# Performance work log

Hardware: AMD Instinct MI355X
Metric: run time of the kernel (lower is better)

The kernel has to match this reference:

```python
import jax, jax.numpy as jnp
import numpy as np

V, E, P, NL, H, I = 50304, 512, 320, 6, 8, 1024
B, S = 2, 1024
HD = P // H            # head_dim = 40
ROT = int(HD * 0.25)   # rotary dims = 10


def layer_norm(x, w, b, eps=1e-5):
    m = jnp.mean(x, -1, keepdims=True)
    v = jnp.mean((x - m) ** 2, -1, keepdims=True)
    return (x - m) * jax.lax.rsqrt(v + eps) * w + b


def setup_inputs() -> dict:
    key = jax.random.key(0)
    ks = jax.random.split(key, 16)
    n = lambda k, s: jax.random.normal(k, s, dtype=jnp.float32) * 0.02
    return dict(
        input_ids=jax.random.randint(ks[0], (B, S), 0, V),
        embed_w=n(ks[1], (V, E)),
        embed_norm_w=jnp.ones((E,)), embed_norm_b=jnp.zeros((E,)),
        dproj_w=n(ks[2], (P + E, P)), dproj_b=jnp.zeros((P,)),
        dproj_ln_w=jnp.ones((P,)), dproj_ln_b=jnp.zeros((P,)),
        ln1_w=jnp.ones((NL, P)), ln1_b=jnp.zeros((NL, P)),
        ln2_w=jnp.ones((NL, P)), ln2_b=jnp.zeros((NL, P)),
        qkv_w=n(ks[3], (NL, P, 3 * P)), qkv_b=jnp.zeros((NL, 3 * P)),
        dense_w=n(ks[4], (NL, P, P)), dense_b=jnp.zeros((NL, P)),
        fc1_w=n(ks[5], (NL, P, I)), fc1_b=jnp.zeros((NL, I)),
        fc2_w=n(ks[6], (NL, I, P)), fc2_b=jnp.zeros((NL, P)),
        final_ln_w=jnp.ones((P,)), final_ln_b=jnp.zeros((P,)),
        lm_head_w=n(ks[7], (V, P)),
    )


def _forward(input_ids, embed_w, embed_norm_w, embed_norm_b, dproj_w, dproj_b,
             dproj_ln_w, dproj_ln_b, ln1_w, ln1_b, ln2_w, ln2_b, qkv_w, qkv_b,
             dense_w, dense_b, fc1_w, fc1_b, fc2_w, fc2_b, final_ln_w, final_ln_b,
             lm_head_w):
    b, s = input_ids.shape
    # 1-2) token embedding + LayerNorm
    te = layer_norm(embed_w[input_ids], embed_norm_w, embed_norm_b)  # [B,S,E]

    # 3) sequential DiverseProjection recurrence over seq_len (lax.scan)
    def step(prev, emb_t):  # prev [B,P], emb_t [B,E]
        h = jnp.concatenate([prev, emb_t], -1) @ dproj_w + dproj_b
        h = jnp.tanh(layer_norm(h, dproj_ln_w, dproj_ln_b))
        return h, h
    _, hs = jax.lax.scan(step, jnp.zeros((b, P), te.dtype), jnp.swapaxes(te, 0, 1))
    x = jnp.swapaxes(hs, 0, 1)  # [B,S,P]

    # RoPE tables (GPT-NeoX style, rotary_pct = 0.25 of head_dim)
    half = ROT // 2
    inv = 1.0 / (10000.0 ** (jnp.arange(0, ROT, 2, dtype=jnp.float32) / ROT))
    freqs = jnp.arange(s, dtype=jnp.float32)[:, None] * inv[None, :]  # [S, ROT/2]
    cos = jnp.cos(jnp.concatenate([freqs, freqs], -1))  # [S, ROT]
    sin = jnp.sin(jnp.concatenate([freqs, freqs], -1))

    def rope(t):  # t: [B,H,S,ROT]
        t1, t2 = t[..., :half], t[..., half:]
        return t * cos + jnp.concatenate([-t2, t1], -1) * sin

    mask = jnp.tril(jnp.ones((s, s), dtype=bool))
    scale = 1.0 / np.sqrt(HD)
    # 4) Pythia (GPT-NeoX) layers: parallel residual attn + mlp
    for l in range(NL):
        a_in = layer_norm(x, ln1_w[l], ln1_b[l])
        qkv = (a_in @ qkv_w[l] + qkv_b[l]).reshape(b, s, H, 3 * HD)
        q, k, v = (jnp.swapaxes(t, 1, 2) for t in jnp.split(qkv, 3, axis=-1))  # [B,H,S,HD]
        q = jnp.concatenate([rope(q[..., :ROT]), q[..., ROT:]], -1)
        k = jnp.concatenate([rope(k[..., :ROT]), k[..., ROT:]], -1)
        scores = jnp.einsum('bhqd,bhkd->bhqk', q, k) * scale
        attn = jax.nn.softmax(jnp.where(mask, scores, jnp.float32(-1e9)), axis=-1)
        ctx = jnp.einsum('bhqk,bhkd->bhqd', attn, v)
        attn_out = jnp.swapaxes(ctx, 1, 2).reshape(b, s, P) @ dense_w[l] + dense_b[l]
        m_in = layer_norm(x, ln2_w[l], ln2_b[l])
        mlp_out = jax.nn.gelu(m_in @ fc1_w[l] + fc1_b[l]) @ fc2_w[l] + fc2_b[l]
        x = x + attn_out + mlp_out
    # 5-6) final LN + LM head (no bias)
    x = layer_norm(x, final_ln_w, final_ln_b)
    return x @ lm_head_w.T  # [B,S,V]


def reference(input_ids, embed_w, embed_norm_w, embed_norm_b, dproj_w, dproj_b,
              dproj_ln_w, dproj_ln_b, ln1_w, ln1_b, ln2_w, ln2_b, qkv_w, qkv_b,
              dense_w, dense_b, fc1_w, fc1_b, fc2_w, fc2_b, final_ln_w, final_ln_b,
              lm_head_w):
    return _forward(input_ids, embed_w, embed_norm_w, embed_norm_b, dproj_w, dproj_b,
                    dproj_ln_w, dproj_ln_b, ln1_w, ln1_b, ln2_w, ln2_b, qkv_w, qkv_b,
                    dense_w, dense_b, fc1_w, fc1_b, fc2_w, fc2_b, final_ln_w,
                    final_ln_b, lm_head_w)
```

## Files before the change

### kernel.cpp

```cpp
#include <hip/hip_runtime.h>

#define VV 50304
#define EE 512
#define PP 320
#define NL 6
#define NH 8
#define II 1024
#define BB 2
#define SS 1024
#define HDD 40

typedef __attribute__((ext_vector_type(8))) __bf16 bf16x8;
typedef __attribute__((ext_vector_type(4))) float f32x4;

__device__ __forceinline__ float gelu_tanh(float x) {
    float x3 = x * x * x;
    return 0.5f * x * (1.f + tanhf(0.7978845608028654f * (x + 0.044715f * x3)));
}

template<int CTRL>
__device__ __forceinline__ float dpp_reduce_add(float v) {
    int s = __builtin_amdgcn_update_dpp(0, __builtin_bit_cast(int, v), CTRL, 0xF, 0xF, true);
    return v + __builtin_bit_cast(float, s);
}
#define DPPRED16(x) do { \
    x = dpp_reduce_add<0xB1>(x);   \
    x = dpp_reduce_add<0x4E>(x);   \
    x = dpp_reduce_add<0x141>(x);  \
    x = dpp_reduce_add<0x140>(x);  \
} while (0)

__global__ __launch_bounds__(64) void embed_ln_kernel(
    const int* __restrict__ ids, const float* __restrict__ embed,
    const float* __restrict__ w, const float* __restrict__ b, float* __restrict__ out)
{
    int r = blockIdx.x;
    int lane = threadIdx.x;
    long id = ids[r];
    const float* xr = embed + id * (long)EE;
    float vals[8];
    float s = 0.f;
#pragma unroll
    for (int i = 0; i < 8; ++i) { vals[i] = xr[lane + i * 64]; s += vals[i]; }
#pragma unroll
    for (int m = 32; m >= 1; m >>= 1) s += __shfl_xor(s, m);
    float mean = s * (1.f / 512.f);
    float v = 0.f;
#pragma unroll
    for (int i = 0; i < 8; ++i) { float d = vals[i] - mean; v += d * d; }
#pragma unroll
    for (int m = 32; m >= 1; m >>= 1) v += __shfl_xor(v, m);
    float rstd = rsqrtf(v * (1.f / 512.f) + 1e-5f);
    float* orow = out + (long)r * EE;
#pragma unroll
    for (int i = 0; i < 8; ++i) {
        int c = lane + i * 64;
        orow[c] = (vals[i] - mean) * rstd * w[c] + b[c];
    }
}

__global__ __launch_bounds__(64) void ln_kernel(
    const float* __restrict__ x, const float* __restrict__ w,
    const float* __restrict__ b, float* __restrict__ out, int N)
{
    int r = blockIdx.x, lane = threadIdx.x;
    const float* xr = x + (long)r * N;
    float s = 0.f;
    for (int i = lane; i < N; i += 64) s += xr[i];
#pragma unroll
    for (int m = 32; m >= 1; m >>= 1) s += __shfl_xor(s, m);
    float mean = s / (float)N;
    float v = 0.f;
    for (int i = lane; i < N; i += 64) { float d = xr[i] - mean; v += d * d; }
#pragma unroll
    for (int m = 32; m >= 1; m >>= 1) v += __shfl_xor(v, m);
    float rstd = rsqrtf(v / (float)N + 1e-5f);
    float* orow = out + (long)r * N;
    for (int i = lane; i < N; i += 64) orow[i] = (xr[i] - mean) * rstd * w[i] + b[i];
}

__global__ __launch_bounds__(256) void gemm_kernel(
    const float* __restrict__ A, const float* __restrict__ B,
    const float* __restrict__ bias, float* __restrict__ C,
    int M, int N, int K, int BT, int act,
    const float* __restrict__ add1, const float* __restrict__ add2)
{
    __shared__ __align__(16) __bf16 As[64 * 40];
    __shared__ __align__(16) __bf16 Bs[64 * 40];
    int tid  = threadIdx.x;
    int lane = tid & 63;
    int wv   = tid >> 6;
    int l15  = lane & 15, quad = lane >> 4;
    int bm = blockIdx.y * 64, bn = blockIdx.x * 64;
    int wm = (wv >> 1) * 32, wn = (wv & 1) * 32;
    f32x4 acc[2][2] = {};

    int sm = tid >> 2;
    int sk = (tid & 3) * 8;
    int bk_n = tid & 63;
    int bk_k = (tid >> 6) * 8;

    for (int k0 = 0; k0 < K; k0 += 32) {
        {
            const float* ap = A + (long)(bm + sm) * K + k0 + sk;
            float4 a0 = *(const float4*)ap;
            float4 a1 = *(const float4*)(ap + 4);
            bf16x8 av;
            av[0] = (__bf16)a0.x; av[1] = (__bf16)a0.y; av[2] = (__bf16)a0.z; av[3] = (__bf16)a0.w;
            av[4] = (__bf16)a1.x; av[5] = (__bf16)a1.y; av[6] = (__bf16)a1.z; av[7] = (__bf16)a1.w;
            *(bf16x8*)&As[sm * 40 + sk] = av;
        }
        if (BT == 0) {
            const float* bp = B + (long)(k0 + bk_k) * N + bn + bk_n;
            bf16x8 bv;
#pragma unroll
            for (int i = 0; i < 8; ++i) bv[i] = (__bf16)bp[(long)i * N];
            *(bf16x8*)&Bs[bk_n * 40 + bk_k] = bv;
        } else {
            const float* bp = B + (long)(bn + sm) * K + k0 + sk;
            float4 b0 = *(const float4*)bp;
            float4 b1 = *(const float4*)(bp + 4);
            bf16x8 bv;
            bv[0] = (__bf16)b0.x; bv[1] = (__bf16)b0.y; bv[2] = (__bf16)b0.z; bv[3] = (__bf16)b0.w;
            bv[4] = (__bf16)b1.x; bv[5] = (__bf16)b1.y; bv[6] = (__bf16)b1.z; bv[7] = (__bf16)b1.w;
            *(bf16x8*)&Bs[sm * 40 + sk] = bv;
        }
        __syncthreads();
#pragma unroll
        for (int mt = 0; mt < 2; ++mt) {
            bf16x8 af = *(const bf16x8*)&As[(wm + mt * 16 + l15) * 40 + quad * 8];
#pragma unroll
            for (int nt = 0; nt < 2; ++nt) {
                bf16x8 bfr = *(const bf16x8*)&Bs[(wn + nt * 16 + l15) * 40 + quad * 8];
                acc[mt][nt] = __builtin_amdgcn_mfma_f32_16x16x32_bf16(af, bfr, acc[mt][nt], 0, 0, 0);
            }
        }
        __syncthreads();
    }
#pragma unroll
    for (int mt = 0; mt < 2; ++mt)
#pragma unroll
    for (int nt = 0; nt < 2; ++nt)
#pragma unroll
    for (int r = 0; r < 4; ++r) {
        int grow = bm + wm + mt * 16 + quad * 4 + r;
        int gcol = bn + wn + nt * 16 + l15;
        float v = acc[mt][nt][r];
        if (bias) v += bias[gcol];
        if (act == 1) v = gelu_tanh(v);
        long idx = (long)grow * N + gcol;
        if (add1) v += add1[idx];
        if (add2) v += add2[idx];
        C[idx] = v;
    }
}

__global__ __launch_bounds__(256, 1) void scan_kernel(
    const float* __restrict__ Wtop,
    const float* __restrict__ c,
    const float* __restrict__ lnw, const float* __restrict__ lnb,
    float* __restrict__ x)
{
    __shared__ __align__(16) __bf16 hA[16 * 328];
    __shared__ __align__(16) float yb2[PP * 2];
    __shared__ __align__(16) float red[16];

    int tid = threadIdx.x;
    int lane = tid & 63;
    int w = tid >> 6;
    int l15 = lane & 15, quad = lane >> 4;

    for (int i = tid; i < 16 * 328; i += 256) hA[i] = (__bf16)0.f;

    bf16x8 bw[5][10];
#pragma unroll
    for (int nt = 0; nt < 5; ++nt) {
        int nn = w * 80 + nt * 16 + l15;
#pragma unroll
        for (int kt = 0; kt < 10; ++kt) {
#pragma unroll
            for (int j = 0; j < 8; ++j) {
                int kk = kt * 32 + quad * 8 + j;
                bw[nt][kt][j] = (__bf16)Wtop[(long)kk * PP + nn];
            }
        }
    }

    int nv = (tid < 128) ? 3 : 2;
    int vb[3], vcol[3];
    vb[0] = 0;            vcol[0] = tid;
    vb[1] = (tid >= 64);  vcol[1] = vb[1] ? (tid - 64) : (tid + 256);
    vb[2] = 1;            vcol[2] = tid + 192;
    float lwv[3], lbv[3];
    long xbase[3]; int ybo[3], hao[3];
#pragma unroll
    for (int i = 0; i < 3; ++i) {
        if (i < nv) {
            lwv[i] = lnw[vcol[i]]; lbv[i] = lnb[vcol[i]];
            xbase[i] = (long)vb[i] * SS * PP + vcol[i];
            ybo[i] = vcol[i] * 2 + vb[i];
            hao[i] = vb[i] * 328 + vcol[i];
        }
    }

    int ccol = w * 80 + l15;
    const float* cp0 = c + ccol;
    const float* cp1 = c + (long)SS * PP + ccol;
    float cc0[5], cc1[5];
#pragma unroll
    for (int nt = 0; nt < 5; ++nt) { cc0[nt] = cp0[nt * 16]; cc1[nt] = cp1[nt * 16]; }
    __syncthreads();

    for (int t = 0; t < SS; ++t) {
        int tn = (t + 1 < SS) ? (t + 1) : t;
        float nc0[5], nc1[5];
#pragma unroll
        for (int nt = 0; nt < 5; ++nt) {
            nc0[nt] = cp0[(long)tn * PP + nt * 16];
            nc1[nt] = cp1[(long)tn * PP + nt * 16];
        }

        f32x4 acc[5] = {};
#pragma unroll
        for (int kt = 0; kt < 10; ++kt) {
            bf16x8 a = *(const bf16x8*)&hA[l15 * 328 + kt * 32 + quad * 8];
#pragma unroll
            for (int nt = 0; nt < 5; ++nt)
                acc[nt] = __builtin_amdgcn_mfma_f32_16x16x32_bf16(a, bw[nt][kt], acc[nt], 0, 0, 0);
        }

        float ya[5], yc[5];
#pragma unroll
        for (int nt = 0; nt < 5; ++nt) { ya[nt] = acc[nt][0] + cc0[nt]; yc[nt] = acc[nt][1] + cc1[nt]; }
        float s10 = ya[0] + ya[1] + ya[2] + ya[3] + ya[4];
        float s20 = ya[0]*ya[0] + ya[1]*ya[1] + ya[2]*ya[2] + ya[3]*ya[3] + ya[4]*ya[4];
        float s11 = yc[0] + yc[1] + yc[2] + yc[3] + yc[4];
        float s21 = yc[0]*yc[0] + yc[1]*yc[1] + yc[2]*yc[2] + yc[3]*yc[3] + yc[4]*yc[4];
        DPPRED16(s10); DPPRED16(s20); DPPRED16(s11); DPPRED16(s21);
        if (quad == 0) {
#pragma unroll
            for (int nt = 0; nt < 5; ++nt) {
                float2 p; p.x = ya[nt]; p.y = yc[nt];
                *(float2*)&yb2[(w * 80 + nt * 16 + l15) * 2] = p;
            }
        }
        if (lane == 0) {
            f32x4 r; r[0] = s10; r[1] = s20; r[2] = s11; r[3] = s21;
            *(f32x4*)&red[w * 4] = r;
        }
        __syncthreads();

        f32x4 r0 = *(const f32x4*)&red[0];
        f32x4 r1 = *(const f32x4*)&red[4];
        f32x4 r2 = *(const f32x4*)&red[8];
        f32x4 r3 = *(const f32x4*)&red[12];
        float S10 = r0[0] + r1[0] + r2[0] + r3[0];
        float S20 = r0[1] + r1[1] + r2[1] + r3[1];
        float S11 = r0[2] + r1[2] + r2[2] + r3[2];
        float S21 = r0[3] + r1[3] + r2[3] + r3[3];
        float mean0 = S10 * (1.f / 320.f), mean1 = S11 * (1.f / 320.f);
        float rstd0 = rsqrtf(S20 * (1.f / 320.f) - mean0 * mean0 + 1e-5f);
        float rstd1 = rsqrtf(S21 * (1.f / 320.f) - mean1 * mean1 + 1e-5f);

#pragma unroll
        for (int i = 0; i < 3; ++i) {
            if (i < nv) {
                float y = yb2[ybo[i]];
                float m  = vb[i] ? mean1 : mean0;
                float rs = vb[i] ? rstd1 : rstd0;
                float z = (y - m) * rs * lwv[i] + lbv[i];
                z = fminf(fmaxf(z, -15.f), 15.f);
                float e = __expf(2.f * z);
                float h = (e - 1.f) / (e + 1.f);
                x[xbase[i] + (long)t * PP] = h;
                hA[hao[i]] = (__bf16)h;
            }
        }
#pragma unroll
        for (int nt = 0; nt < 5; ++nt) { cc0[nt] = nc0[nt]; cc1[nt] = nc1[nt]; }
        __syncthreads();
    }
}

__global__ __launch_bounds__(256) void rope_kernel(float* __restrict__ qkv)
{
    int t = blockIdx.x * 256 + threadIdx.x;
    if (t >= BB * SS * NH) return;
    int h = t & 7;
    int s = (t >> 3) & (SS - 1);
    int b = t >> 13;
    float* p = qkv + ((long)(b * SS + s)) * 960 + h * 120;
    const float inv[5] = {1.f, 0.158489319f, 0.0251188643f, 0.00398107171f, 0.000630957344f};
    float* q = p;
    float* k = p + HDD;
#pragma unroll
    for (int i = 0; i < 5; ++i) {
        float ang = (float)s * inv[i];
        float sn, cs;
        sincosf(ang, &sn, &cs);
        float q1 = q[i], q2 = q[i + 5];
        q[i]     = q1 * cs - q2 * sn;
        q[i + 5] = q2 * cs + q1 * sn;
        float k1 = k[i], k2 = k[i + 5];
        k[i]     = k1 * cs - k2 * sn;
        k[i + 5] = k2 * cs + k1 * sn;
    }
}

__global__ __launch_bounds__(256) void attn_kernel(
    const float* __restrict__ qkv, float* __restrict__ ctx)
{
    int qt = blockIdx.x & 15;
    int h  = (blockIdx.x >> 4) & 7;
    int b  = blockIdx.x >> 7;
    int tid = threadIdx.x;
    __shared__ float Qs[64][41], Ks[64][41], Vs[64][41];
    __shared__ float Ss[64][65];
    __shared__ float mS[64], lS[64], aS[64];
    const float scale = 0.15811388300841897f;
    long base = (long)b * SS * 960 + h * 120;
    int q0 = qt * 64;

    for (int i = tid; i < 64 * HDD; i += 256) {
        int r = i / HDD, d = i % HDD;
        Qs[r][d] = qkv[base + (long)(q0 + r) * 960 + d] * scale;
    }
    if (tid < 64) { mS[tid] = -1e30f; lS[tid] = 0.f; }
    float O[10];
#pragma unroll
    for (int i = 0; i < 10; ++i) O[i] = 0.f;
    int qo = tid >> 2, dg = (tid & 3) * 10;
    int sq = tid >> 2, sk16 = (tid & 3) * 16;
    __syncthreads();

    for (int kt = 0; kt <= qt; ++kt) {
        int k0 = kt * 64;
        for (int i = tid; i < 64 * HDD; i += 256) {
            int r = i / HDD, d = i % HDD;
            Ks[r][d] = qkv[base + (long)(k0 + r) * 960 + HDD + d];
            Vs[r][d] = qkv[base + (long)(k0 + r) * 960 + 2 * HDD + d];
        }
        __syncthreads();
#pragma unroll 1
        for (int kk = 0; kk < 16; ++kk) {
            int kcol = sk16 + kk;
            float s = 0.f;
#pragma unroll
            for (int d = 0; d < HDD; ++d) s += Qs[sq][d] * Ks[kcol][d];
            if (k0 + kcol > q0 + sq) s = -1e9f;
            Ss[sq][kcol] = s;
        }
        __syncthreads();
        if (tid < 64) {
            float mOld = mS[tid];
            float mNew = mOld;
            for (int j = 0; j < 64; ++j) mNew = fmaxf(mNew, Ss[tid][j]);
            float alpha = __expf(mOld - mNew);
            float psum = 0.f;
            for (int j = 0; j < 64; ++j) {
                float p = __expf(Ss[tid][j] - mNew);
                Ss[tid][j] = p;
                psum += p;
            }
            lS[tid] = lS[tid] * alpha + psum;
            mS[tid] = mNew;
            aS[tid] = alpha;
        }
        __syncthreads();
        float alpha = aS[qo];
#pragma unroll
        for (int i = 0; i < 10; ++i) O[i] *= alpha;
        for (int k = 0; k < 64; ++k) {
            float p = Ss[qo][k];
#pragma unroll
            for (int i = 0; i < 10; ++i) O[i] += p * Vs[k][dg + i];
        }
        __syncthreads();
    }
    float linv = 1.f / lS[qo];
#pragma unroll
    for (int i = 0; i < 10; ++i)
        ctx[((long)(b * SS + q0 + qo)) * PP + h * HDD + dg + i] = O[i] * linv;
}

extern "C" void kernel_launch(void* const* d_in, const int* in_sizes, int n_in,
                              void* d_out, int out_size, void* d_ws, size_t ws_size,
                              hipStream_t stream)
{
    (void)in_sizes; (void)n_in; (void)out_size; (void)ws_size;
    const int*   ids       = (const int*)d_in[0];
    const float* embed_w   = (const float*)d_in[1];
    const float* embed_nw  = (const float*)d_in[2];
    const float* embed_nb  = (const float*)d_in[3];
    const float* dproj_w   = (const float*)d_in[4];
    const float* dproj_b   = (const float*)d_in[5];
    const float* dproj_lnw = (const float*)d_in[6];
    const float* dproj_lnb = (const float*)d_in[7];
    const float* ln1_w     = (const float*)d_in[8];
    const float* ln1_b     = (const float*)d_in[9];
    const float* ln2_w     = (const float*)d_in[10];
    const float* ln2_b     = (const float*)d_in[11];
    const float* qkv_w     = (const float*)d_in[12];
    const float* qkv_b     = (const float*)d_in[13];
    const float* dense_w   = (const float*)d_in[14];
    const float* dense_b   = (const float*)d_in[15];
    const float* fc1_w     = (const float*)d_in[16];
    const float* fc1_b     = (const float*)d_in[17];
    const float* fc2_w     = (const float*)d_in[18];
    const float* fc2_b     = (const float*)d_in[19];
    const float* fln_w     = (const float*)d_in[20];
    const float* fln_b     = (const float*)d_in[21];
    const float* lm_w      = (const float*)d_in[22];
    float* out = (float*)d_out;
    float* ws  = (float*)d_ws;

    const long R = (long)BB * SS;
    float* te    = ws;
    float* cbuf  = te   + 1048576;
    float* x     = cbuf + 655360;
    float* lnbuf = x    + 655360;
    float* qkv   = lnbuf + 655360;
    float* ctx   = qkv  + 1966080;
    float* attn  = ctx  + 655360;
    float* mlp1  = attn + 655360;

    embed_ln_kernel<<<R, 64, 0, stream>>>(ids, embed_w, embed_nw, embed_nb, te);
    gemm_kernel<<<dim3(PP / 64, R / 64), 256, 0, stream>>>(
        te, dproj_w + (long)PP * PP, dproj_b, cbuf, R, PP, EE, 0, 0, nullptr, nullptr);
    scan_kernel<<<1, 256, 0, stream>>>(dproj_w, cbuf, dproj_lnw, dproj_lnb, x);

    for (int l = 0; l < NL; ++l) {
        ln_kernel<<<R, 64, 0, stream>>>(x, ln1_w + l * PP, ln1_b + l * PP, lnbuf, PP);
        gemm_kernel<<<dim3(960 / 64, R / 64), 256, 0, stream>>>(
            lnbuf, qkv_w + (long)l * PP * 960, qkv_b + l * 960, qkv, R, 960, PP, 0, 0, nullptr, nullptr);
        rope_kernel<<<(BB * SS * NH + 255) / 256, 256, 0, stream>>>(qkv);
        attn_kernel<<<BB * NH * 16, 256, 0, stream>>>(qkv, ctx);
        gemm_kernel<<<dim3(PP / 64, R / 64), 256, 0, stream>>>(
            ctx, dense_w + (long)l * PP * PP, dense_b + l * PP, attn, R, PP, PP, 0, 0, nullptr, nullptr);
        ln_kernel<<<R, 64, 0, stream>>>(x, ln2_w + l * PP, ln2_b + l * PP, lnbuf, PP);
        gemm_kernel<<<dim3(II / 64, R / 64), 256, 0, stream>>>(
            lnbuf, fc1_w + (long)l * PP * II, fc1_b + l * II, mlp1, R, II, PP, 0, 1, nullptr, nullptr);
        gemm_kernel<<<dim3(PP / 64, R / 64), 256, 0, stream>>>(
            mlp1, fc2_w + (long)l * II * PP, fc2_b + l * PP, x, R, PP, II, 0, 0, x, attn);
    }
    ln_kernel<<<R, 64, 0, stream>>>(x, fln_w, fln_b, lnbuf, PP);
    gemm_kernel<<<dim3(VV / 64, R / 64), 256, 0, stream>>>(
        lnbuf, lm_w, nullptr, out, R, VV, PP, 1, 0, nullptr, nullptr);
}
```

Before: 4.312 ms.

## Stage scan inputs via async LDS loads and batch output writes in chunks

```diff
diff --git a/kernel.cpp b/kernel.cpp
--- a/kernel.cpp
+++ b/kernel.cpp
@@ -12,6 +12,9 @@
 
 typedef __attribute__((ext_vector_type(8))) __bf16 bf16x8;
 typedef __attribute__((ext_vector_type(4))) float f32x4;
+
+#define GLOBAL_AS __attribute__((address_space(1)))
+#define LDS_AS __attribute__((address_space(3)))
 
 __device__ __forceinline__ float gelu_tanh(float x) {
     float x3 = x * x * x;
@@ -155,6 +158,7 @@
     }
 }
 
+#define CH 4
 __global__ __launch_bounds__(256, 1) void scan_kernel(
     const float* __restrict__ Wtop,
     const float* __restrict__ c,
@@ -162,8 +166,9 @@
     float* __restrict__ x)
 {
     __shared__ __align__(16) __bf16 hA[16 * 328];
-    __shared__ __align__(16) float yb2[PP * 2];
     __shared__ __align__(16) float red[16];
+    __shared__ __align__(16) float cbuf[2][CH * 640];
+    __shared__ __align__(16) float xh[CH * 640];
 
     int tid = threadIdx.x;
     int lane = tid & 63;
@@ -186,47 +191,77 @@
         }
     }
 
-    int nv = (tid < 128) ? 3 : 2;
-    int vb[3], vcol[3];
-    vb[0] = 0;            vcol[0] = tid;
-    vb[1] = (tid >= 64);  vcol[1] = vb[1] ? (tid - 64) : (tid + 256);
-    vb[2] = 1;            vcol[2] = tid + 192;
-    float lwv[3], lbv[3];
-    long xbase[3]; int ybo[3], hao[3];
-#pragma unroll
-    for (int i = 0; i < 3; ++i) {
-        if (i < nv) {
-            lwv[i] = lnw[vcol[i]]; lbv[i] = lnb[vcol[i]];
-            xbase[i] = (long)vb[i] * SS * PP + vcol[i];
-            ybo[i] = vcol[i] * 2 + vb[i];
-            hao[i] = vb[i] * 328 + vcol[i];
-        }
-    }
-
-    int ccol = w * 80 + l15;
-    const float* cp0 = c + ccol;
-    const float* cp1 = c + (long)SS * PP + ccol;
-    float cc0[5], cc1[5];
-#pragma unroll
-    for (int nt = 0; nt < 5; ++nt) { cc0[nt] = cp0[nt * 16]; cc1[nt] = cp1[nt * 16]; }
+    float lw[5], lb[5];
+#pragma unroll
+    for (int nt = 0; nt < 5; ++nt) {
+        int col = w * 80 + nt * 16 + l15;
+        lw[nt] = lnw[col]; lb[nt] = lnb[col];
+    }
+
+    const float4* c4 = (const float4*)c;
+    auto stage_chunk = [&](int k, int buf) {
+#pragma unroll
+        for (int i = 0; i < 3; ++i) {
+            int sl = i * 64 + lane;
+            if (sl < 160) {
+                int slot = w * 160 + sl;
+                int region = slot / 320, idx = slot % 320;
+                const float4* src = c4 + ((long)region * (SS * 80) + (long)k * 320 + idx);
+                LDS_AS void* dst = (LDS_AS void*)((LDS_AS char*)(LDS_AS float*)&cbuf[buf][0]
+                                                  + (long)(w * 160 + i * 64) * 16);
+                __builtin_amdgcn_global_load_lds((const GLOBAL_AS void*)src, dst, 16, 0, 0);
+            }
+        }
+    };
+    stage_chunk(0, 0);
+    stage_chunk(1, 1);
     __syncthreads();
 
+    const __bf16* arow = &hA[l15 * 328 + quad * 8];
+
     for (int t = 0; t < SS; ++t) {
-        int tn = (t + 1 < SS) ? (t + 1) : t;
-        float nc0[5], nc1[5];
+        int tt = t & (CH - 1);
+        int cb = (t >> 2) & 1;
+
+        if (tt == 0 && t > 0) {
+            int t0 = t - CH;
+            int j0 = tid, j1 = tid + 256, j2 = tid + 512;
+            {
+                float4 v0 = *(const float4*)&xh[j0 * 4];
+                int b0 = j0 / 320, r0 = j0 % 320;
+                *(float4*)&x[((long)b0 * SS + (t0 + r0 / 80)) * PP + (r0 % 80) * 4] = v0;
+                float4 v1 = *(const float4*)&xh[j1 * 4];
+                int b1 = j1 / 320, r1 = j1 % 320;
+                *(float4*)&x[((long)b1 * SS + (t0 + r1 / 80)) * PP + (r1 % 80) * 4] = v1;
+                if (tid < 128) {
+                    float4 v2 = *(const float4*)&xh[j2 * 4];
+                    int b2 = j2 / 320, r2 = j2 % 320;
+                    *(float4*)&x[((long)b2 * SS + (t0 + r2 / 80)) * PP + (r2 % 80) * 4] = v2;
+                }
+            }
+            int kn = (t >> 2) + 1;
+            if (kn < SS / CH) stage_chunk(kn, kn & 1);
+        }
+
+        float cc0[5], cc1[5];
 #pragma unroll
         for (int nt = 0; nt < 5; ++nt) {
-            nc0[nt] = cp0[(long)tn * PP + nt * 16];
-            nc1[nt] = cp1[(long)tn * PP + nt * 16];
+            int col = w * 80 + nt * 16 + l15;
+            cc0[nt] = cbuf[cb][tt * 320 + col];
+            cc1[nt] = cbuf[cb][(CH + tt) * 320 + col];
         }
 
         f32x4 acc[5] = {};
+        bf16x8 a_cur = *(const bf16x8*)&arow[0];
 #pragma unroll
         for (int kt = 0; kt < 10; ++kt) {
-            bf16x8 a = *(const bf16x8*)&hA[l15 * 328 + kt * 32 + quad * 8];
-#pragma unroll
-            for (int nt = 0; nt < 5; ++nt)
-                acc[nt] = __builtin_amdgcn_mfma_f32_16x16x32_bf16(a, bw[nt][kt], acc[nt], 0, 0, 0);
+            bf16x8 a_nxt = *(const bf16x8*)&arow[(kt < 9 ? kt + 1 : 9) * 32];
+            acc[0] = __builtin_amdgcn_mfma_f32_16x16x32_bf16(a_cur, bw[0][kt], acc[0], 0, 0, 0);
+            acc[1] = __builtin_amdgcn_mfma_f32_16x16x32_bf16(a_cur, bw[1][kt], acc[1], 0, 0, 0);
+            acc[2] = __builtin_amdgcn_mfma_f32_16x16x32_bf16(a_cur, bw[2][kt], acc[2], 0, 0, 0);
+            acc[3] = __builtin_amdgcn_mfma_f32_16x16x32_bf16(a_cur, bw[3][kt], acc[3], 0, 0, 0);
+            acc[4] = __builtin_amdgcn_mfma_f32_16x16x32_bf16(a_cur, bw[4][kt], acc[4], 0, 0, 0);
+            a_cur = a_nxt;
         }
 
         float ya[5], yc[5];
@@ -237,13 +272,6 @@
         float s11 = yc[0] + yc[1] + yc[2] + yc[3] + yc[4];
         float s21 = yc[0]*yc[0] + yc[1]*yc[1] + yc[2]*yc[2] + yc[3]*yc[3] + yc[4]*yc[4];
         DPPRED16(s10); DPPRED16(s20); DPPRED16(s11); DPPRED16(s21);
-        if (quad == 0) {
-#pragma unroll
-            for (int nt = 0; nt < 5; ++nt) {
-                float2 p; p.x = ya[nt]; p.y = yc[nt];
-                *(float2*)&yb2[(w * 80 + nt * 16 + l15) * 2] = p;
-            }
-        }
         if (lane == 0) {
             f32x4 r; r[0] = s10; r[1] = s20; r[2] = s11; r[3] = s21;
             *(f32x4*)&red[w * 4] = r;
@@ -262,23 +290,41 @@
         float rstd0 = rsqrtf(S20 * (1.f / 320.f) - mean0 * mean0 + 1e-5f);
         float rstd1 = rsqrtf(S21 * (1.f / 320.f) - mean1 * mean1 + 1e-5f);
 
-#pragma unroll
-        for (int i = 0; i < 3; ++i) {
-            if (i < nv) {
-                float y = yb2[ybo[i]];
-                float m  = vb[i] ? mean1 : mean0;
-                float rs = vb[i] ? rstd1 : rstd0;
-                float z = (y - m) * rs * lwv[i] + lbv[i];
-                z = fminf(fmaxf(z, -15.f), 15.f);
-                float e = __expf(2.f * z);
-                float h = (e - 1.f) / (e + 1.f);
-                x[xbase[i] + (long)t * PP] = h;
-                hA[hao[i]] = (__bf16)h;
-            }
-        }
-#pragma unroll
-        for (int nt = 0; nt < 5; ++nt) { cc0[nt] = nc0[nt]; cc1[nt] = nc1[nt]; }
-        __syncthreads();
+        if (quad == 0) {
+#pragma unroll
+            for (int nt = 0; nt < 5; ++nt) {
+                int col = w * 80 + nt * 16 + l15;
+                float z0 = (ya[nt] - mean0) * rstd0 * lw[nt] + lb[nt];
+                z0 = fminf(fmaxf(z0, -15.f), 15.f);
+                float e0 = __expf(2.f * z0);
+                float h0 = (e0 - 1.f) / (e0 + 1.f);
+                float z1 = (yc[nt] - mean1) * rstd1 * lw[nt] + lb[nt];
+                z1 = fminf(fmaxf(z1, -15.f), 15.f);
+                float e1 = __expf(2.f * z1);
+                float h1 = (e1 - 1.f) / (e1 + 1.f);
+                hA[col]       = (__bf16)h0;
+                hA[328 + col] = (__bf16)h1;
+                xh[tt * 320 + col]        = h0;
+                xh[(CH + tt) * 320 + col] = h1;
+            }
+        }
+        __syncthreads();
+    }
+
+    {
+        int t0 = SS - CH;
+        int j0 = tid, j1 = tid + 256, j2 = tid + 512;
+        float4 v0 = *(const float4*)&xh[j0 * 4];
+        int b0 = j0 / 320, r0 = j0 % 320;
+        *(float4*)&x[((long)b0 * SS + (t0 + r0 / 80)) * PP + (r0 % 80) * 4] = v0;
+        float4 v1 = *(const float4*)&xh[j1 * 4];
+        int b1 = j1 / 320, r1 = j1 % 320;
+        *(float4*)&x[((long)b1 * SS + (t0 + r1 / 80)) * PP + (r1 % 80) * 4] = v1;
+        if (tid < 128) {
+            float4 v2 = *(const float4*)&xh[j2 * 4];
+            int b2 = j2 / 320, r2 = j2 % 320;
+            *(float4*)&x[((long)b2 * SS + (t0 + r2 / 80)) * PP + (r2 % 80) * 4] = v2;
+        }
     }
 }
 
```

New measurement: 4.495 ms. 4.2% more time.
